# Performance work log

Measured on AMD Instinct MI355X. Metric: run time of the kernel, lower is better.

The kernel has to match this reference:

```python
import jax, jax.numpy as jnp
import numpy as np

N, E, B, D, R, L = 60000, 600000, 512, 128, 30, 3
CUT_LOW, CUT_HIGH = 0.0, 10.0
N_ATOM_TYPES = 100


def _sp(x, beta, threshold):
    # torch.nn.Softplus(beta, threshold): x if beta*x > threshold else log1p(exp(beta*x))/beta
    bx = beta * x
    return jnp.where(bx > threshold, x, jnp.log1p(jnp.exp(jnp.minimum(bx, threshold))) / beta)


def setup_inputs() -> dict:
    key = jax.random.key(0)
    ks = jax.random.split(key, 16)

    def lin(k, fi, fo):
        k1, k2 = jax.random.split(k)
        W = jax.random.normal(k1, (fi, fo), jnp.float32) * (fi ** -0.5)
        b = jax.random.normal(k2, (fo,), jnp.float32) * 0.01
        return W, b

    def lin_stack(k, fi, fo, n):
        Ws, bs = zip(*[lin(kk, fi, fo) for kk in jax.random.split(k, n)])
        return jnp.stack(Ws), jnp.stack(bs)

    inp = {}
    inp['atom_type'] = jax.random.randint(ks[0], (N,), 0, N_ATOM_TYPES)
    inp['src'] = jax.random.randint(ks[1], (E,), 0, N)
    inp['dst'] = jax.random.randint(ks[2], (E,), 0, N)
    inp['graph_ids'] = jnp.sort(jax.random.randint(ks[3], (N,), 0, B))
    inp['dist'] = jax.random.uniform(ks[4], (E,), jnp.float32) * CUT_HIGH
    inp['node_emb'] = jax.random.normal(ks[5], (N_ATOM_TYPES, D), jnp.float32) * 0.1
    inp['W_n1'], inp['b_n1'] = lin_stack(ks[6], D, D, L)
    inp['W_c1'], inp['b_c1'] = lin_stack(ks[7], R, D, L)
    inp['W_c2'], inp['b_c2'] = lin_stack(ks[8], D, D, L)
    inp['W_c3'], inp['b_c3'] = lin_stack(ks[9], D, D, L)
    inp['W_n2'], inp['b_n2'] = lin_stack(ks[10], D, D, L)
    inp['W_n3'], inp['b_n3'] = lin_stack(ks[11], D, D, L)
    inp['W_r1'], inp['b_r1'] = lin(ks[12], D * (L + 1), 64)
    inp['W_r2'], inp['b_r2'] = lin(ks[13], 64, 1)
    return inp


def reference(atom_type, src, dst, graph_ids, dist, node_emb,
              W_n1, b_n1, W_c1, b_c1, W_c2, b_c2, W_c3, b_c3,
              W_n2, b_n2, W_n3, b_n3, W_r1, b_r1, W_r2, b_r2):
    # RBF expansion of edge distances: exp(-(d - mu_k)^2 / gap)  -> [E, R]
    centers = jnp.linspace(CUT_LOW, CUT_HIGH, R).astype(dist.dtype)
    gap = centers[1] - centers[0]
    rbf = jnp.exp(-((dist[:, None] - centers) ** 2) / gap)

    h = node_emb[atom_type]  # node embedding lookup [N, D]
    hs = [h]
    for i in range(L):  # MultiLevelInteraction layers (fixed small count)
        h_new = hs[-1] @ W_n1[i] + b_n1[i]                       # node_layer1 [N, D]
        # VEConv edge MLP on rbf (linear1 -> softplus(0.5,14) -> linear2 -> linear3)
        e = _sp(rbf @ W_c1[i] + b_c1[i], 0.5, 14.0) @ W_c2[i] + b_c2[i]
        e = e @ W_c3[i] + b_c3[i]                                 # [E, D]
        # sum_e(h_new[src]*e) + sum_e(e) fused into one scatter-sum over dst
        msg = (h_new[src] + 1.0) * e                              # [E, D]
        node = jax.ops.segment_sum(msg, dst, num_segments=N)      # [N, D]
        new_node = _sp(node @ W_n2[i] + b_n2[i], 0.5, 14.0) @ W_n3[i] + b_n3[i]
        hs.append(hs[-1] + new_node)                              # residual h_i
    hcat = jnp.concatenate(hs, axis=1)                            # [N, D*(L+1)]
    out = _sp(hcat @ W_r1 + b_r1, 1.0, 20.0) @ W_r2 + b_r2        # [N, 1]
    # dgl.sum_nodes per molecule, then flatten -> [B]
    return jax.ops.segment_sum(out[:, 0], graph_ids, num_segments=B)
```

## Files before the change

kernel.cpp:

```cpp
#include <hip/hip_runtime.h>
#include <math.h>

#define N_NODES 60000
#define N_EDGES 600000
#define B_GRAPHS 512
#define DIM 128
#define RBF_R 30
#define NLAYERS 3
#define NBINS 1024
#define CHUNK 512
#define NCHUNK ((N_NODES + CHUNK - 1) / CHUNK)
#define NTILES (N_NODES / 16)

#define NB_CONV 704
#define NB_EMBED 30000
#define NB_TABLE (3 * NBINS)

typedef __attribute__((ext_vector_type(8))) short bf16x8;
typedef __attribute__((ext_vector_type(4))) float f32x4;

__device__ __forceinline__ float sp05(float x) {
    float bx = 0.5f * x;
    return bx > 14.0f ? x : 2.0f * log1pf(expf(bx));
}
__device__ __forceinline__ float sp1(float x) {
    return x > 20.0f ? x : log1pf(expf(x));
}
__device__ __forceinline__ unsigned short f2bf(float f) {
    unsigned int u = __float_as_uint(f);
    unsigned int r = u + 0x7FFFu + ((u >> 16) & 1u);
    return (unsigned short)(r >> 16);
}
__device__ __forceinline__ float bf2f(unsigned int s) {
    return __uint_as_float(s << 16);
}

__device__ __forceinline__ size_t hidx(int row, int col) {
    return (size_t)((row >> 4) * 2048 + (col >> 5) * 512 +
                    ((((col >> 3) & 3) << 4) + (row & 15)) * 8 + (col & 7));
}

__global__ __launch_bounds__(256) void k_setup(
    const float* __restrict__ Wn1, const float* __restrict__ Wn2,
    const float* __restrict__ Wn3, const float* __restrict__ Wr1,
    const int* __restrict__ atom_type, const float* __restrict__ node_emb,
    const float* __restrict__ Wc1, const float* __restrict__ bc1,
    const float* __restrict__ Wc2, const float* __restrict__ bc2,
    const float* __restrict__ Wc3, const float* __restrict__ bc3,
    unsigned short* __restrict__ WtF, unsigned short* __restrict__ Wr1tF,
    unsigned short* __restrict__ hb0, unsigned int* __restrict__ packed) {
    int b = blockIdx.x;
    int tid = threadIdx.x;
    if (b < NB_CONV) {
        int i = b * 256 + tid;
        if (i < 9 * 16384) {
            int mat = i >> 14, r = i & 16383;
            int frag = r >> 9, within = r & 511;
            int ks = frag >> 3, ntile = frag & 7;
            int lane = within >> 3, j = within & 7;
            int q = lane >> 4, l16 = lane & 15;
            int n = ntile * 16 + l16;
            int k = ks * 32 + q * 8 + j;
            const float* src = (mat < 3) ? (Wn1 + (size_t)mat * 16384)
                             : (mat < 6) ? (Wn2 + (size_t)(mat - 3) * 16384)
                                         : (Wn3 + (size_t)(mat - 6) * 16384);
            WtF[i] = f2bf(src[k * 128 + n]);
        } else {
            int ii = i - 9 * 16384;
            int frag = ii >> 9, within = ii & 511;
            int lvl = frag >> 4, ks = (frag >> 2) & 3, ntile = frag & 3;
            int lane = within >> 3, j = within & 7;
            int q = lane >> 4, l16 = lane & 15;
            int n = ntile * 16 + l16;
            int k = lvl * 128 + ks * 32 + q * 8 + j;
            Wr1tF[ii] = f2bf(Wr1[k * 64 + n]);
        }
        return;
    }
    if (b < NB_CONV + NB_EMBED) {
        int i = (b - NB_CONV) * 256 + tid;
        int tile = i >> 11;
        int rem = i & 2047;
        int ks = rem >> 9;
        int lane = (rem >> 3) & 63;
        int j = rem & 7;
        int row = tile * 16 + (lane & 15);
        int col = ks * 32 + (lane >> 4) * 8 + j;
        hb0[i] = f2bf(node_emb[atom_type[row] * DIM + col]);
        return;
    }
    {
        __shared__ float t[2][DIM];
        __shared__ float u[2][DIM];
        __shared__ float va[2][DIM];
        int idx = b - NB_CONV - NB_EMBED;
        int lyr = idx / NBINS;
        int bin = idx % NBINS;
        int half = tid >> 7;
        int d = tid & 127;
        const float* wc1 = Wc1 + (size_t)lyr * RBF_R * DIM;
        const float* wc2 = Wc2 + (size_t)lyr * DIM * DIM;
        const float* wc3 = Wc3 + (size_t)lyr * DIM * DIM;
        float dist = (float)(bin + half) * (10.0f / (float)NBINS);
        const float gap = 10.0f / 29.0f;
        float acc = bc1[lyr * DIM + d];
#pragma unroll
        for (int k = 0; k < RBF_R; ++k) {
            float c = (float)k * (10.0f / 29.0f);
            float df = dist - c;
            acc += expf(-df * df / gap) * wc1[k * DIM + d];
        }
        t[half][d] = sp05(acc);
        __syncthreads();
        acc = bc2[lyr * DIM + d];
#pragma unroll 8
        for (int k = 0; k < DIM; ++k) acc += t[half][k] * wc2[k * DIM + d];
        u[half][d] = acc;
        __syncthreads();
        acc = bc3[lyr * DIM + d];
#pragma unroll 8
        for (int k = 0; k < DIM; ++k) acc += u[half][k] * wc3[k * DIM + d];
        va[half][d] = acc;
        __syncthreads();
        if (half == 0) {
            float a = bf2f(f2bf(va[0][d]));
            float bv = bf2f(f2bf(va[1][d]));
            packed[((size_t)lyr * NBINS + bin) * DIM + d] =
                (unsigned int)f2bf(a) | ((unsigned int)f2bf(bv - a) << 16);
        }
    }
}


__global__ void k_hist(const int* __restrict__ dst, int* __restrict__ counts) {
    int e = blockIdx.x * blockDim.x + threadIdx.x;
    if (e >= N_EDGES) return;
    atomicAdd(&counts[dst[e]], 1);
}

__global__ void k_bsum(const int* __restrict__ counts, int* __restrict__ bsums) {
    __shared__ int red[256];
    int c = blockIdx.x, tid = threadIdx.x;
    int base = c * CHUNK;
    int v = 0;
    for (int i = tid; i < CHUNK; i += 256)
        if (base + i < N_NODES) v += counts[base + i];
    red[tid] = v;
    __syncthreads();
    for (int s = 128; s > 0; s >>= 1) {
        if (tid < s) red[tid] += red[tid + s];
        __syncthreads();
    }
    if (tid == 0) bsums[c] = red[0];
}

__global__ void k_scan_b(int* __restrict__ bsums) {
    __shared__ int sb[NCHUNK];
    int tid = threadIdx.x;
    if (tid < NCHUNK) sb[tid] = bsums[tid];
    __syncthreads();
    if (tid == 0) {
        int run = 0;
        for (int i = 0; i < NCHUNK; ++i) { int v = sb[i]; sb[i] = run; run += v; }
    }
    __syncthreads();
    if (tid < NCHUNK) bsums[tid] = sb[tid];
}

__global__ void k_scan_final(const int* __restrict__ counts, const int* __restrict__ bsums,
                             int* __restrict__ offsets) {
    __shared__ int sc[CHUNK];
    int c = blockIdx.x, tid = threadIdx.x;
    int base = c * CHUNK;
    for (int i = tid; i < CHUNK; i += 256)
        sc[i] = (base + i < N_NODES) ? counts[base + i] : 0;
    __syncthreads();
    if (tid == 0) {
        int run = bsums[c];
        for (int i = 0; i < CHUNK; ++i) { int v = sc[i]; sc[i] = run; run += v; }
    }
    __syncthreads();
    for (int i = tid; i < CHUNK; i += 256)
        if (base + i < N_NODES) offsets[base + i] = sc[i];
    if (c == 0 && tid == 0) offsets[N_NODES] = N_EDGES;
}

__global__ void k_fill(const int* __restrict__ src, const int* __restrict__ dst,
                       const float* __restrict__ dist,
                       const int* __restrict__ offsets, int* __restrict__ cnt2,
                       uint2* __restrict__ meta) {
    int e = blockIdx.x * blockDim.x + threadIdx.x;
    if (e >= N_EDGES) return;
    int d = dst[e];
    int pos = offsets[d] + atomicAdd(&cnt2[d], 1);
    float x = dist[e];
    float p = x * ((float)NBINS / 10.0f);
    int bin = (int)p;
    if (bin > NBINS - 1) bin = NBINS - 1;
    float w = p - (float)bin;
    int wq = (int)(w * 65535.0f + 0.5f);
    if (wq > 65535) wq = 65535;
    meta[pos] = make_uint2((unsigned)src[e], ((unsigned)bin << 16) | (unsigned)wq);
}


__global__ __launch_bounds__(256) void k_gemm_g(const unsigned short* __restrict__ Ab,
                                                const unsigned short* __restrict__ WtF,
                                                const float* __restrict__ bias,
                                                unsigned short* __restrict__ Cb) {
    int tid = threadIdx.x;
    int wave = tid >> 6, lane = tid & 63;
    int q = lane >> 4, l16 = lane & 15;
    int mhalf = wave & 1, nhalf = wave >> 1;
    int rb = blockIdx.x * 64 + mhalf * 32;
    int c0 = nhalf * 64;
    bf16x8 bfrag[4][4];
#pragma unroll
    for (int ks = 0; ks < 4; ++ks)
#pragma unroll
        for (int nt = 0; nt < 4; ++nt)
            bfrag[ks][nt] = *(const bf16x8*)&WtF[(size_t)(ks * 8 + nhalf * 4 + nt) * 512 + lane * 8];
    f32x4 acc[2][4] = {};
#pragma unroll
    for (int ks = 0; ks < 4; ++ks)
#pragma unroll
        for (int mt = 0; mt < 2; ++mt) {
            int tt = (rb >> 4) + mt;
            if (tt > NTILES - 1) tt = NTILES - 1;
            bf16x8 a = *(const bf16x8*)&Ab[(size_t)tt * 2048 + ks * 512 + lane * 8];
#pragma unroll
            for (int nt = 0; nt < 4; ++nt)
                acc[mt][nt] = __builtin_amdgcn_mfma_f32_16x16x32_bf16(a, bfrag[ks][nt], acc[mt][nt], 0, 0, 0);
        }
#pragma unroll
    for (int mt = 0; mt < 2; ++mt)
#pragma unroll
        for (int nt = 0; nt < 4; ++nt) {
            int col = c0 + nt * 16 + l16;
            float b = bias[col] + 1.0f;
#pragma unroll
            for (int r = 0; r < 4; ++r) {
                int row = rb + mt * 16 + q * 4 + r;
                if (row < N_NODES) Cb[(size_t)row * 128 + col] = f2bf(acc[mt][nt][r] + b);
            }
        }
}

__global__ __launch_bounds__(256) void k_gather(
    const int* __restrict__ offsets, const uint2* __restrict__ meta,
    const unsigned int* __restrict__ packed, const unsigned short* __restrict__ gb,
    unsigned short* __restrict__ nodeb) {
    int wave = threadIdx.x >> 6, lane = threadIdx.x & 63;
    int n = blockIdx.x * 4 + wave;
    int beg = offsets[n], end = offsets[n + 1];
    int off = lane * 2;
    const float ws = 1.0f / 65535.0f;
    float acc0 = 0.f, acc1 = 0.f, acc2 = 0.f, acc3 = 0.f;
    int j = beg;
    for (; j + 8 <= end; j += 8) {
        uint2 m[8];
        uint2 p[8];
        unsigned int g[8];
#pragma unroll
        for (int e = 0; e < 8; ++e) m[e] = meta[j + e];
#pragma unroll
        for (int e = 0; e < 8; ++e) {
            p[e] = *(const uint2*)&packed[(size_t)(m[e].y >> 16) * DIM + off];
            g[e] = *(const unsigned int*)&gb[(size_t)m[e].x * DIM + off];
        }
#pragma unroll
        for (int e = 0; e < 8; e += 2) {
            float w0 = (float)(m[e].y & 0xffff) * ws;
            float w1 = (float)(m[e + 1].y & 0xffff) * ws;
            acc0 += bf2f(g[e] & 0xffff)     * (bf2f(p[e].x & 0xffff)     + w0 * bf2f(p[e].x >> 16));
            acc1 += bf2f(g[e] >> 16)        * (bf2f(p[e].y & 0xffff)     + w0 * bf2f(p[e].y >> 16));
            acc2 += bf2f(g[e + 1] & 0xffff) * (bf2f(p[e + 1].x & 0xffff) + w1 * bf2f(p[e + 1].x >> 16));
            acc3 += bf2f(g[e + 1] >> 16)    * (bf2f(p[e + 1].y & 0xffff) + w1 * bf2f(p[e + 1].y >> 16));
        }
    }
    for (; j + 2 <= end; j += 2) {
        uint2 m0 = meta[j], m1 = meta[j + 1];
        uint2 p0 = *(const uint2*)&packed[(size_t)(m0.y >> 16) * DIM + off];
        uint2 p1 = *(const uint2*)&packed[(size_t)(m1.y >> 16) * DIM + off];
        unsigned int g0 = *(const unsigned int*)&gb[(size_t)m0.x * DIM + off];
        unsigned int g1 = *(const unsigned int*)&gb[(size_t)m1.x * DIM + off];
        float w0 = (float)(m0.y & 0xffff) * ws;
        float w1 = (float)(m1.y & 0xffff) * ws;
        acc0 += bf2f(g0 & 0xffff) * (bf2f(p0.x & 0xffff) + w0 * bf2f(p0.x >> 16));
        acc1 += bf2f(g0 >> 16)    * (bf2f(p0.y & 0xffff) + w0 * bf2f(p0.y >> 16));
        acc2 += bf2f(g1 & 0xffff) * (bf2f(p1.x & 0xffff) + w1 * bf2f(p1.x >> 16));
        acc3 += bf2f(g1 >> 16)    * (bf2f(p1.y & 0xffff) + w1 * bf2f(p1.y >> 16));
    }
    if (j < end) {
        uint2 m0 = meta[j];
        uint2 p0 = *(const uint2*)&packed[(size_t)(m0.y >> 16) * DIM + off];
        unsigned int g0 = *(const unsigned int*)&gb[(size_t)m0.x * DIM + off];
        float w0 = (float)(m0.y & 0xffff) * ws;
        acc0 += bf2f(g0 & 0xffff) * (bf2f(p0.x & 0xffff) + w0 * bf2f(p0.x >> 16));
        acc1 += bf2f(g0 >> 16)    * (bf2f(p0.y & 0xffff) + w0 * bf2f(p0.y >> 16));
    }
    acc0 += acc2; acc1 += acc3;
    unsigned int o = (unsigned int)f2bf(acc0) | ((unsigned int)f2bf(acc1) << 16);
    *(unsigned int*)&nodeb[(size_t)n * DIM + off] = o;
}

__global__ __launch_bounds__(256) void k_node_update(
    const unsigned short* __restrict__ nodeb,
    const unsigned short* __restrict__ W2tF, const float* __restrict__ b2,
    const unsigned short* __restrict__ W3tF, const float* __restrict__ b3,
    const unsigned short* __restrict__ hb_in, unsigned short* __restrict__ hb_out,
    const unsigned short* __restrict__ WgF, const float* __restrict__ bg,
    unsigned short* __restrict__ gb, int do_g) {
    __shared__ unsigned short ts[64][136];
    __shared__ unsigned short hs[64][136];
    int tid = threadIdx.x;
    int wave = tid >> 6, lane = tid & 63;
    int q = lane >> 4, l16 = lane & 15;
    int mhalf = wave & 1, nhalf = wave >> 1;
    int rb = blockIdx.x * 64 + mhalf * 32;
    int c0 = nhalf * 64;

    bf16x8 bfrag[4][4];
#pragma unroll
    for (int ks = 0; ks < 4; ++ks)
#pragma unroll
        for (int nt = 0; nt < 4; ++nt)
            bfrag[ks][nt] = *(const bf16x8*)&W2tF[(size_t)(ks * 8 + nhalf * 4 + nt) * 512 + lane * 8];
    f32x4 acc[2][4] = {};
#pragma unroll
    for (int ks = 0; ks < 4; ++ks)
#pragma unroll
        for (int mt = 0; mt < 2; ++mt) {
            int m = rb + mt * 16 + l16;
            if (m > N_NODES - 1) m = N_NODES - 1;
            bf16x8 a = *(const bf16x8*)&nodeb[(size_t)m * 128 + ks * 32 + q * 8];
#pragma unroll
            for (int nt = 0; nt < 4; ++nt)
                acc[mt][nt] = __builtin_amdgcn_mfma_f32_16x16x32_bf16(a, bfrag[ks][nt], acc[mt][nt], 0, 0, 0);
        }
#pragma unroll
    for (int mt = 0; mt < 2; ++mt)
#pragma unroll
        for (int nt = 0; nt < 4; ++nt) {
            int col = c0 + nt * 16 + l16;
            float b = b2[col];
#pragma unroll
            for (int r = 0; r < 4; ++r) {
                int lrow = mhalf * 32 + mt * 16 + q * 4 + r;
                ts[lrow][col] = f2bf(sp05(acc[mt][nt][r] + b));
            }
        }
    __syncthreads();
#pragma unroll
    for (int ks = 0; ks < 4; ++ks)
#pragma unroll
        for (int nt = 0; nt < 4; ++nt)
            bfrag[ks][nt] = *(const bf16x8*)&W3tF[(size_t)(ks * 8 + nhalf * 4 + nt) * 512 + lane * 8];
#pragma unroll
    for (int mt = 0; mt < 2; ++mt)
#pragma unroll
        for (int nt = 0; nt < 4; ++nt) acc[mt][nt] = (f32x4){0.f, 0.f, 0.f, 0.f};
#pragma unroll
    for (int ks = 0; ks < 4; ++ks)
#pragma unroll
        for (int mt = 0; mt < 2; ++mt) {
            int lrow = mhalf * 32 + mt * 16 + l16;
            bf16x8 a = *(const bf16x8*)&ts[lrow][ks * 32 + q * 8];
#pragma unroll
            for (int nt = 0; nt < 4; ++nt)
                acc[mt][nt] = __builtin_amdgcn_mfma_f32_16x16x32_bf16(a, bfrag[ks][nt], acc[mt][nt], 0, 0, 0);
        }
#pragma unroll
    for (int mt = 0; mt < 2; ++mt)
#pragma unroll
        for (int nt = 0; nt < 4; ++nt) {
            int col = c0 + nt * 16 + l16;
            float b = b3[col];
#pragma unroll
            for (int r = 0; r < 4; ++r) {
                int row = rb + mt * 16 + q * 4 + r;
                int lrow = mhalf * 32 + mt * 16 + q * 4 + r;
                if (row < N_NODES) {
                    size_t idx = hidx(row, col);
                    float v = bf2f(hb_in[idx]) + acc[mt][nt][r] + b;
                    unsigned short bf = f2bf(v);
                    hb_out[idx] = bf;
                    hs[lrow][col] = bf;
                } else {
                    hs[lrow][col] = 0;
                }
            }
        }
    if (!do_g) return;
    __syncthreads();
#pragma unroll
    for (int ks = 0; ks < 4; ++ks)
#pragma unroll
        for (int nt = 0; nt < 4; ++nt)
            bfrag[ks][nt] = *(const bf16x8*)&WgF[(size_t)(ks * 8 + nhalf * 4 + nt) * 512 + lane * 8];
#pragma unroll
    for (int mt = 0; mt < 2; ++mt)
#pragma unroll
        for (int nt = 0; nt < 4; ++nt) acc[mt][nt] = (f32x4){0.f, 0.f, 0.f, 0.f};
#pragma unroll
    for (int ks = 0; ks < 4; ++ks)
#pragma unroll
        for (int mt = 0; mt < 2; ++mt) {
            int lrow = mhalf * 32 + mt * 16 + l16;
            bf16x8 a = *(const bf16x8*)&hs[lrow][ks * 32 + q * 8];
#pragma unroll
            for (int nt = 0; nt < 4; ++nt)
                acc[mt][nt] = __builtin_amdgcn_mfma_f32_16x16x32_bf16(a, bfrag[ks][nt], acc[mt][nt], 0, 0, 0);
        }
#pragma unroll
    for (int mt = 0; mt < 2; ++mt)
#pragma unroll
        for (int nt = 0; nt < 4; ++nt) {
            int col = c0 + nt * 16 + l16;
            float b = bg[col] + 1.0f;
#pragma unroll
            for (int r = 0; r < 4; ++r) {
                int row = rb + mt * 16 + q * 4 + r;
                if (row < N_NODES) gb[(size_t)row * 128 + col] = f2bf(acc[mt][nt][r] + b);
            }
        }
}

__global__ __launch_bounds__(256, 1) void k_readout(
    const unsigned short* __restrict__ hb0, const unsigned short* __restrict__ hb1,
    const unsigned short* __restrict__ hb2, const unsigned short* __restrict__ hb3,
    const unsigned short* __restrict__ Wr1tF, const float* __restrict__ br1,
    const float* __restrict__ Wr2, const float* __restrict__ br2,
    const int* __restrict__ graph_ids, float* __restrict__ out) {
    int tid = threadIdx.x;
    int wave = tid >> 6, lane = tid & 63;
    int q = lane >> 4, l16 = lane & 15;
    int rb0 = blockIdx.x * 128 + wave * 16;
    int tt0 = blockIdx.x * 8 + wave;
    int tt1 = tt0 + 4;
    if (tt0 > NTILES - 1) tt0 = NTILES - 1;
    if (tt1 > NTILES - 1) tt1 = NTILES - 1;

    bf16x8 a[4][2][4];
    const unsigned short* hbs[4] = {hb0, hb1, hb2, hb3};
#pragma unroll
    for (int lvl = 0; lvl < 4; ++lvl) {
        const unsigned short* Ab = hbs[lvl];
#pragma unroll
        for (int ks = 0; ks < 4; ++ks) {
            a[lvl][0][ks] = *(const bf16x8*)&Ab[(size_t)tt0 * 2048 + ks * 512 + lane * 8];
            a[lvl][1][ks] = *(const bf16x8*)&Ab[(size_t)tt1 * 2048 + ks * 512 + lane * 8];
        }
    }
    asm volatile("" ::: "memory");
    f32x4 acc[2][4] = {};
#pragma unroll
    for (int lvl = 0; lvl < 4; ++lvl) {
        bf16x8 bfrag[4][4];
#pragma unroll
        for (int ks = 0; ks < 4; ++ks)
#pragma unroll
            for (int nt = 0; nt < 4; ++nt)
                bfrag[ks][nt] = *(const bf16x8*)&Wr1tF[(size_t)((lvl * 4 + ks) * 4 + nt) * 512 + lane * 8];
#pragma unroll
        for (int ks = 0; ks < 4; ++ks)
#pragma unroll
            for (int mt = 0; mt < 2; ++mt)
#pragma unroll
                for (int nt = 0; nt < 4; ++nt)
                    acc[mt][nt] = __builtin_amdgcn_mfma_f32_16x16x32_bf16(a[lvl][mt][ks], bfrag[ks][nt], acc[mt][nt], 0, 0, 0);
    }
    float brr = br2[0];
#pragma unroll
    for (int mt = 0; mt < 2; ++mt) {
        float partial[4] = {0.f, 0.f, 0.f, 0.f};
#pragma unroll
        for (int nt = 0; nt < 4; ++nt) {
            int col = nt * 16 + l16;
            float b = br1[col];
            float w = Wr2[col];
#pragma unroll
            for (int r = 0; r < 4; ++r) partial[r] += sp1(acc[mt][nt][r] + b) * w;
        }
#pragma unroll
        for (int r = 0; r < 4; ++r) {
            float v = partial[r];
            v += __shfl_xor(v, 1); v += __shfl_xor(v, 2);
            v += __shfl_xor(v, 4); v += __shfl_xor(v, 8);
            if (l16 == 0) {
                int row = rb0 + mt * 64 + q * 4 + r;
                if (row < N_NODES) atomicAdd(&out[graph_ids[row]], v + brr);
            }
        }
    }
}

extern "C" void kernel_launch(void* const* d_in, const int* in_sizes, int n_in,
                              void* d_out, int out_size, void* d_ws, size_t ws_size,
                              hipStream_t stream) {
    const int* atom_type   = (const int*)d_in[0];
    const int* src         = (const int*)d_in[1];
    const int* dst         = (const int*)d_in[2];
    const int* graph_ids   = (const int*)d_in[3];
    const float* dist      = (const float*)d_in[4];
    const float* node_emb  = (const float*)d_in[5];
    const float* W_n1 = (const float*)d_in[6];  const float* b_n1 = (const float*)d_in[7];
    const float* W_c1 = (const float*)d_in[8];  const float* b_c1 = (const float*)d_in[9];
    const float* W_c2 = (const float*)d_in[10]; const float* b_c2 = (const float*)d_in[11];
    const float* W_c3 = (const float*)d_in[12]; const float* b_c3 = (const float*)d_in[13];
    const float* W_n2 = (const float*)d_in[14]; const float* b_n2 = (const float*)d_in[15];
    const float* W_n3 = (const float*)d_in[16]; const float* b_n3 = (const float*)d_in[17];
    const float* W_r1 = (const float*)d_in[18]; const float* b_r1 = (const float*)d_in[19];
    const float* W_r2 = (const float*)d_in[20]; const float* b_r2 = (const float*)d_in[21];
    float* out = (float*)d_out;

    size_t ND = (size_t)N_NODES * DIM;
    uint2* meta   = (uint2*)d_ws;
    int* offsets  = (int*)(meta + N_EDGES);
    int* counts   = offsets + 60008;
    int* cnt2     = counts + N_NODES;
    int* bsums    = cnt2 + N_NODES;
    unsigned int* packed = (unsigned int*)(bsums + 128);
    unsigned short* hb0    = (unsigned short*)(packed + (size_t)3 * NBINS * DIM);
    unsigned short* hb1    = hb0 + ND;
    unsigned short* hb2    = hb1 + ND;
    unsigned short* hb3    = hb2 + ND;
    unsigned short* gb     = hb3 + ND;
    unsigned short* nodeb  = gb + ND;
    unsigned short* WtF    = nodeb + ND;
    unsigned short* Wr1tF  = WtF + 9 * 16384;

    unsigned short* hbp[4] = {hb0, hb1, hb2, hb3};

    hipMemsetAsync(out, 0, B_GRAPHS * sizeof(float), stream);
    hipMemsetAsync(counts, 0, (2 * N_NODES + 128) * sizeof(int), stream);

    k_setup<<<NB_CONV + NB_EMBED + NB_TABLE, 256, 0, stream>>>(
        W_n1, W_n2, W_n3, W_r1, atom_type, node_emb,
        W_c1, b_c1, W_c2, b_c2, W_c3, b_c3,
        WtF, Wr1tF, hb0, packed);

    k_hist<<<(N_EDGES + 255) / 256, 256, 0, stream>>>(dst, counts);
    k_bsum<<<NCHUNK, 256, 0, stream>>>(counts, bsums);
    k_scan_b<<<1, 128, 0, stream>>>(bsums);
    k_scan_final<<<NCHUNK, 256, 0, stream>>>(counts, bsums, offsets);
    k_fill<<<(N_EDGES + 255) / 256, 256, 0, stream>>>(src, dst, dist, offsets, cnt2, meta);

    int gblocks = (N_NODES + 63) / 64;
    int rblocks = (N_NODES + 127) / 128;
    k_gemm_g<<<gblocks, 256, 0, stream>>>(hb0, WtF, b_n1, gb);
    for (int i = 0; i < NLAYERS; ++i) {
        k_gather<<<N_NODES / 4, 256, 0, stream>>>(
            offsets, meta, packed + (size_t)i * NBINS * DIM, gb, nodeb);
        int do_g = (i < NLAYERS - 1) ? 1 : 0;
        k_node_update<<<gblocks, 256, 0, stream>>>(
            nodeb, WtF + (size_t)(3 + i) * 16384, b_n2 + (size_t)i * DIM,
            WtF + (size_t)(6 + i) * 16384, b_n3 + (size_t)i * DIM,
            hbp[i], hbp[i + 1],
            WtF + (size_t)(i + 1) * 16384, b_n1 + (size_t)(i + 1 < 3 ? i + 1 : 0) * DIM,
            gb, do_g);
    }
    k_readout<<<rblocks, 256, 0, stream>>>(
        hb0, hb1, hb2, hb3, Wr1tF, b_r1, W_r2, b_r2, graph_ids, out);
}
```

Before: 580.0 us.

## Fuse readout MLP into final node-update kernel, skip writing last hidden state

The separate readout kernel is removed. The last layer's node-update kernel now runs the readout: it takes the final hidden state from shared memory and reads the three earlier levels from global memory. This saves one launch and avoids writing and re-reading hb3. In exchange the node-update kernel carries more registers and code, and readout work is spread over 64-row blocks with one 16-row tile per wave, where the old readout used 128-row blocks.

```diff
diff --git a/kernel.cpp b/kernel.cpp
--- a/kernel.cpp
+++ b/kernel.cpp
@@ -310,7 +310,12 @@
     const unsigned short* __restrict__ W3tF, const float* __restrict__ b3,
     const unsigned short* __restrict__ hb_in, unsigned short* __restrict__ hb_out,
     const unsigned short* __restrict__ WgF, const float* __restrict__ bg,
-    unsigned short* __restrict__ gb, int do_g) {
+    unsigned short* __restrict__ gb, int do_g, int do_ro,
+    const unsigned short* __restrict__ r0, const unsigned short* __restrict__ r1,
+    const unsigned short* __restrict__ r2,
+    const unsigned short* __restrict__ Wr1tF, const float* __restrict__ br1,
+    const float* __restrict__ Wr2, const float* __restrict__ br2,
+    const int* __restrict__ graph_ids, float* __restrict__ out) {
     __shared__ unsigned short ts[64][136];
     __shared__ unsigned short hs[64][136];
     int tid = threadIdx.x;
@@ -384,113 +389,107 @@
                     size_t idx = hidx(row, col);
                     float v = bf2f(hb_in[idx]) + acc[mt][nt][r] + b;
                     unsigned short bf = f2bf(v);
-                    hb_out[idx] = bf;
+                    if (!do_ro) hb_out[idx] = bf;
                     hs[lrow][col] = bf;
                 } else {
                     hs[lrow][col] = 0;
                 }
             }
         }
-    if (!do_g) return;
-    __syncthreads();
-#pragma unroll
-    for (int ks = 0; ks < 4; ++ks)
-#pragma unroll
-        for (int nt = 0; nt < 4; ++nt)
-            bfrag[ks][nt] = *(const bf16x8*)&WgF[(size_t)(ks * 8 + nhalf * 4 + nt) * 512 + lane * 8];
-#pragma unroll
-    for (int mt = 0; mt < 2; ++mt)
-#pragma unroll
-        for (int nt = 0; nt < 4; ++nt) acc[mt][nt] = (f32x4){0.f, 0.f, 0.f, 0.f};
-#pragma unroll
-    for (int ks = 0; ks < 4; ++ks)
-#pragma unroll
-        for (int mt = 0; mt < 2; ++mt) {
-            int lrow = mhalf * 32 + mt * 16 + l16;
-            bf16x8 a = *(const bf16x8*)&hs[lrow][ks * 32 + q * 8];
-#pragma unroll
-            for (int nt = 0; nt < 4; ++nt)
-                acc[mt][nt] = __builtin_amdgcn_mfma_f32_16x16x32_bf16(a, bfrag[ks][nt], acc[mt][nt], 0, 0, 0);
-        }
-#pragma unroll
-    for (int mt = 0; mt < 2; ++mt)
-#pragma unroll
-        for (int nt = 0; nt < 4; ++nt) {
-            int col = c0 + nt * 16 + l16;
-            float b = bg[col] + 1.0f;
-#pragma unroll
-            for (int r = 0; r < 4; ++r) {
-                int row = rb + mt * 16 + q * 4 + r;
-                if (row < N_NODES) gb[(size_t)row * 128 + col] = f2bf(acc[mt][nt][r] + b);
+    if (do_g) {
+        __syncthreads();
+#pragma unroll
+        for (int ks = 0; ks < 4; ++ks)
+#pragma unroll
+            for (int nt = 0; nt < 4; ++nt)
+                bfrag[ks][nt] = *(const bf16x8*)&WgF[(size_t)(ks * 8 + nhalf * 4 + nt) * 512 + lane * 8];
+#pragma unroll
+        for (int mt = 0; mt < 2; ++mt)
+#pragma unroll
+            for (int nt = 0; nt < 4; ++nt) acc[mt][nt] = (f32x4){0.f, 0.f, 0.f, 0.f};
+#pragma unroll
+        for (int ks = 0; ks < 4; ++ks)
+#pragma unroll
+            for (int mt = 0; mt < 2; ++mt) {
+                int lrow = mhalf * 32 + mt * 16 + l16;
+                bf16x8 a = *(const bf16x8*)&hs[lrow][ks * 32 + q * 8];
+#pragma unroll
+                for (int nt = 0; nt < 4; ++nt)
+                    acc[mt][nt] = __builtin_amdgcn_mfma_f32_16x16x32_bf16(a, bfrag[ks][nt], acc[mt][nt], 0, 0, 0);
             }
-        }
-}
-
-__global__ __launch_bounds__(256, 1) void k_readout(
-    const unsigned short* __restrict__ hb0, const unsigned short* __restrict__ hb1,
-    const unsigned short* __restrict__ hb2, const unsigned short* __restrict__ hb3,
-    const unsigned short* __restrict__ Wr1tF, const float* __restrict__ br1,
-    const float* __restrict__ Wr2, const float* __restrict__ br2,
-    const int* __restrict__ graph_ids, float* __restrict__ out) {
-    int tid = threadIdx.x;
-    int wave = tid >> 6, lane = tid & 63;
-    int q = lane >> 4, l16 = lane & 15;
-    int rb0 = blockIdx.x * 128 + wave * 16;
-    int tt0 = blockIdx.x * 8 + wave;
-    int tt1 = tt0 + 4;
-    if (tt0 > NTILES - 1) tt0 = NTILES - 1;
-    if (tt1 > NTILES - 1) tt1 = NTILES - 1;
-
-    bf16x8 a[4][2][4];
-    const unsigned short* hbs[4] = {hb0, hb1, hb2, hb3};
-#pragma unroll
-    for (int lvl = 0; lvl < 4; ++lvl) {
-        const unsigned short* Ab = hbs[lvl];
-#pragma unroll
-        for (int ks = 0; ks < 4; ++ks) {
-            a[lvl][0][ks] = *(const bf16x8*)&Ab[(size_t)tt0 * 2048 + ks * 512 + lane * 8];
-            a[lvl][1][ks] = *(const bf16x8*)&Ab[(size_t)tt1 * 2048 + ks * 512 + lane * 8];
-        }
-    }
-    asm volatile("" ::: "memory");
-    f32x4 acc[2][4] = {};
-#pragma unroll
-    for (int lvl = 0; lvl < 4; ++lvl) {
-        bf16x8 bfrag[4][4];
-#pragma unroll
-        for (int ks = 0; ks < 4; ++ks)
-#pragma unroll
-            for (int nt = 0; nt < 4; ++nt)
-                bfrag[ks][nt] = *(const bf16x8*)&Wr1tF[(size_t)((lvl * 4 + ks) * 4 + nt) * 512 + lane * 8];
-#pragma unroll
-        for (int ks = 0; ks < 4; ++ks)
-#pragma unroll
-            for (int mt = 0; mt < 2; ++mt)
-#pragma unroll
-                for (int nt = 0; nt < 4; ++nt)
-                    acc[mt][nt] = __builtin_amdgcn_mfma_f32_16x16x32_bf16(a[lvl][mt][ks], bfrag[ks][nt], acc[mt][nt], 0, 0, 0);
+#pragma unroll
+        for (int mt = 0; mt < 2; ++mt)
+#pragma unroll
+            for (int nt = 0; nt < 4; ++nt) {
+                int col = c0 + nt * 16 + l16;
+                float b = bg[col] + 1.0f;
+#pragma unroll
+                for (int r = 0; r < 4; ++r) {
+                    int row = rb + mt * 16 + q * 4 + r;
+                    if (row < N_NODES) gb[(size_t)row * 128 + col] = f2bf(acc[mt][nt][r] + b);
+                }
+            }
+        return;
+    }
+    if (!do_ro) return;
+    __syncthreads();
+    int tile = blockIdx.x * 4 + wave;
+    int tt = tile > NTILES - 1 ? NTILES - 1 : tile;
+    f32x4 racc[4] = {};
+    const unsigned short* rlv[3] = {r0, r1, r2};
+#pragma unroll
+    for (int lvl = 0; lvl < 3; ++lvl) {
+        bf16x8 af[4];
+#pragma unroll
+        for (int ks = 0; ks < 4; ++ks)
+            af[ks] = *(const bf16x8*)&rlv[lvl][(size_t)tt * 2048 + ks * 512 + lane * 8];
+        bf16x8 rb_[4][4];
+#pragma unroll
+        for (int ks = 0; ks < 4; ++ks)
+#pragma unroll
+            for (int nt = 0; nt < 4; ++nt)
+                rb_[ks][nt] = *(const bf16x8*)&Wr1tF[(size_t)((lvl * 4 + ks) * 4 + nt) * 512 + lane * 8];
+#pragma unroll
+        for (int ks = 0; ks < 4; ++ks)
+#pragma unroll
+            for (int nt = 0; nt < 4; ++nt)
+                racc[nt] = __builtin_amdgcn_mfma_f32_16x16x32_bf16(af[ks], rb_[ks][nt], racc[nt], 0, 0, 0);
+    }
+    {
+        bf16x8 af[4];
+#pragma unroll
+        for (int ks = 0; ks < 4; ++ks)
+            af[ks] = *(const bf16x8*)&hs[wave * 16 + l16][ks * 32 + q * 8];
+        bf16x8 rb_[4][4];
+#pragma unroll
+        for (int ks = 0; ks < 4; ++ks)
+#pragma unroll
+            for (int nt = 0; nt < 4; ++nt)
+                rb_[ks][nt] = *(const bf16x8*)&Wr1tF[(size_t)((3 * 4 + ks) * 4 + nt) * 512 + lane * 8];
+#pragma unroll
+        for (int ks = 0; ks < 4; ++ks)
+#pragma unroll
+            for (int nt = 0; nt < 4; ++nt)
+                racc[nt] = __builtin_amdgcn_mfma_f32_16x16x32_bf16(af[ks], rb_[ks][nt], racc[nt], 0, 0, 0);
     }
     float brr = br2[0];
-#pragma unroll
-    for (int mt = 0; mt < 2; ++mt) {
-        float partial[4] = {0.f, 0.f, 0.f, 0.f};
-#pragma unroll
-        for (int nt = 0; nt < 4; ++nt) {
-            int col = nt * 16 + l16;
-            float b = br1[col];
-            float w = Wr2[col];
-#pragma unroll
-            for (int r = 0; r < 4; ++r) partial[r] += sp1(acc[mt][nt][r] + b) * w;
-        }
-#pragma unroll
-        for (int r = 0; r < 4; ++r) {
-            float v = partial[r];
-            v += __shfl_xor(v, 1); v += __shfl_xor(v, 2);
-            v += __shfl_xor(v, 4); v += __shfl_xor(v, 8);
-            if (l16 == 0) {
-                int row = rb0 + mt * 64 + q * 4 + r;
-                if (row < N_NODES) atomicAdd(&out[graph_ids[row]], v + brr);
-            }
+    float partial[4] = {0.f, 0.f, 0.f, 0.f};
+#pragma unroll
+    for (int nt = 0; nt < 4; ++nt) {
+        int col = nt * 16 + l16;
+        float b = br1[col];
+        float w = Wr2[col];
+#pragma unroll
+        for (int r = 0; r < 4; ++r) partial[r] += sp1(racc[nt][r] + b) * w;
+    }
+#pragma unroll
+    for (int r = 0; r < 4; ++r) {
+        float v = partial[r];
+        v += __shfl_xor(v, 1); v += __shfl_xor(v, 2);
+        v += __shfl_xor(v, 4); v += __shfl_xor(v, 8);
+        if (l16 == 0) {
+            int row = tile * 16 + q * 4 + r;
+            if (row < N_NODES) atomicAdd(&out[graph_ids[row]], v + brr);
         }
     }
 }
@@ -547,19 +546,18 @@
     k_fill<<<(N_EDGES + 255) / 256, 256, 0, stream>>>(src, dst, dist, offsets, cnt2, meta);
 
     int gblocks = (N_NODES + 63) / 64;
-    int rblocks = (N_NODES + 127) / 128;
     k_gemm_g<<<gblocks, 256, 0, stream>>>(hb0, WtF, b_n1, gb);
     for (int i = 0; i < NLAYERS; ++i) {
         k_gather<<<N_NODES / 4, 256, 0, stream>>>(
             offsets, meta, packed + (size_t)i * NBINS * DIM, gb, nodeb);
         int do_g = (i < NLAYERS - 1) ? 1 : 0;
+        int do_ro = (i == NLAYERS - 1) ? 1 : 0;
         k_node_update<<<gblocks, 256, 0, stream>>>(
             nodeb, WtF + (size_t)(3 + i) * 16384, b_n2 + (size_t)i * DIM,
             WtF + (size_t)(6 + i) * 16384, b_n3 + (size_t)i * DIM,
             hbp[i], hbp[i + 1],
             WtF + (size_t)(i + 1) * 16384, b_n1 + (size_t)(i + 1 < 3 ? i + 1 : 0) * DIM,
-            gb, do_g);
-    }
-    k_readout<<<rblocks, 256, 0, stream>>>(
-        hb0, hb1, hb2, hb3, Wr1tF, b_r1, W_r2, b_r2, graph_ids, out);
-}
+            gb, do_g, do_ro,
+            hb0, hb1, hb2, Wr1tF, b_r1, W_r2, b_r2, graph_ids, out);
+    }
+}
```

Result: slower. 593.8 us (+2.4%).
